# Performance work log

Hardware: AMD Instinct MI355X
Metric: run time of the kernel (lower is better)

## Reference

```python
import jax, jax.numpy as jnp
import numpy as np

# Static config mirroring FinalFFTAudioEngine(compression_ratio=0.3)
COMPRESSION_RATIO = 0.3
ENERGY_THRESHOLD = 0.05
WINDOW = 256  # window_size=512 -> power-of-2 loop ends at 512 -> min(512//2, 512) = 256


def _important_mask(energy, min_count, threshold):
    """Threshold mask, replaced by top-k mask if too few survive (faithful to torch code)."""
    th_mask = energy > threshold
    _, idx = jax.lax.top_k(energy, min_count)
    tk_mask = jnp.zeros(energy.shape, dtype=bool).at[idx].set(True)
    return jnp.where(jnp.sum(th_mask) < min_count, tk_mask, th_mask)


def setup_inputs() -> dict:
    key = jax.random.key(0)
    weight_matrix = jax.random.normal(key, (4096, 4096), dtype=jnp.float32)
    return {"weight_matrix": weight_matrix}


def reference(weight_matrix):
    # weight_to_audio_signal: flatten + max-abs normalize
    signal = weight_matrix.reshape(-1).astype(jnp.float32)
    n = signal.shape[0]  # 16777216, exact multiple of WINDOW -> no padding branch
    sig_max = jnp.max(jnp.abs(signal))
    norm = jnp.where(sig_max > 1e-10, sig_max, jnp.float32(1.0))
    signal = signal / norm

    # optimized_spectral_analysis: non-overlapping windows + per-window FFT
    windows = signal.reshape(-1, WINDOW)          # [T, F] = [65536, 256]
    spec = jnp.fft.fft(windows)                   # complex64 [T, F]

    # intelligent_frequency_selection
    energy = jnp.abs(spec) ** 2                   # [T, F]
    freq_energy = jnp.mean(energy, axis=0)        # [F]
    time_energy = jnp.mean(energy, axis=1)        # [T]
    min_freqs = max(1, int(WINDOW * (1.0 - COMPRESSION_RATIO * 0.7)))          # 202
    min_times = max(1, int(windows.shape[0] * (1.0 - COMPRESSION_RATIO * 0.7)))  # 51773
    freq_mask = _important_mask(freq_energy, min_freqs,
                                ENERGY_THRESHOLD * jnp.max(freq_energy))
    time_mask = _important_mask(time_energy, min_times,
                                ENERGY_THRESHOLD * jnp.max(time_energy))

    # lossless_compression: fused masked copy (replaces nested python double-for-loop)
    mask2d = time_mask[:, None] & freq_mask[None, :]
    compressed = jnp.where(mask2d, spec, jnp.zeros((), dtype=spec.dtype))

    # perfect_reconstruction: IFFT, take real part, flatten, trim to original length
    recon = jnp.real(jnp.fft.ifft(compressed)).reshape(-1)[:n]
    return recon
```

## Files before the change

kernel.cpp:

```cpp
#include <hip/hip_runtime.h>

#define N_TOTAL   16777216
#define NWIN      65536
#define MIN_FREQS 202
#define MIN_TIMES 51773
#define NSLOTS    64
#define NBLK      1024

#define IDX_TCNT    2
#define IDX_FMALL   3
#define IDX_TTHR    4
#define IDX_INVNORM 5
#define IDX_FCNT    6
#define IDX_FMASK   8
#define IDX_SLOTS   264
#define IDX_AMAXB   16648
#define IDX_TMAXB   18696
#define IDX_SUMSQ   20744
#define IDX_TMASKA  86280

__device__ __forceinline__ void fft16(float ar[16], float ai[16])
{
#define SWP(a,b) { float t_=ar[a]; ar[a]=ar[b]; ar[b]=t_; \
                   t_=ai[a]; ai[a]=ai[b]; ai[b]=t_; }
    SWP(1,8) SWP(2,4) SWP(3,12) SWP(5,10) SWP(7,14) SWP(11,13)
#undef SWP
#pragma unroll
    for (int i = 0; i < 16; i += 2) {
        float tr = ar[i+1], ti = ai[i+1];
        ar[i+1] = ar[i] - tr; ai[i+1] = ai[i] - ti;
        ar[i] += tr;          ai[i] += ti;
    }
#pragma unroll
    for (int i = 0; i < 16; i += 4) {
        { float tr = ar[i+2], ti = ai[i+2];
          ar[i+2] = ar[i] - tr; ai[i+2] = ai[i] - ti; ar[i] += tr; ai[i] += ti; }
        { float tr = ai[i+3], ti = -ar[i+3];
          ar[i+3] = ar[i+1] - tr; ai[i+3] = ai[i+1] - ti; ar[i+1] += tr; ai[i+1] += ti; }
    }
#pragma unroll
    for (int i = 0; i < 16; i += 8) {
        { float tr = ar[i+4], ti = ai[i+4];
          ar[i+4] = ar[i] - tr; ai[i+4] = ai[i] - ti; ar[i] += tr; ai[i] += ti; }
        { float br = ar[i+5], bi = ai[i+5];
          float tr = 0.70710678f * (br + bi), ti = 0.70710678f * (bi - br);
          ar[i+5] = ar[i+1] - tr; ai[i+5] = ai[i+1] - ti; ar[i+1] += tr; ai[i+1] += ti; }
        { float tr = ai[i+6], ti = -ar[i+6];
          ar[i+6] = ar[i+2] - tr; ai[i+6] = ai[i+2] - ti; ar[i+2] += tr; ai[i+2] += ti; }
        { float br = ar[i+7], bi = ai[i+7];
          float tr = 0.70710678f * (bi - br), ti = -0.70710678f * (br + bi);
          ar[i+7] = ar[i+3] - tr; ai[i+7] = ai[i+3] - ti; ar[i+3] += tr; ai[i+3] += ti; }
    }
    { float tr = ar[8], ti = ai[8];
      ar[8] = ar[0] - tr; ai[8] = ai[0] - ti; ar[0] += tr; ai[0] += ti; }
#define BUT(J, WR, WI) { float br = ar[8+J], bi = ai[8+J];     \
      float tr = br*(WR) - bi*(WI), ti = br*(WI) + bi*(WR);    \
      ar[8+J] = ar[J] - tr; ai[8+J] = ai[J] - ti; ar[J] += tr; ai[J] += ti; }
    BUT(1,  0.92387953f, -0.38268343f)
    BUT(2,  0.70710678f, -0.70710678f)
    BUT(3,  0.38268343f, -0.92387953f)
    BUT(4,  0.f, -1.f)
    BUT(5, -0.38268343f, -0.92387953f)
    BUT(6, -0.70710678f, -0.70710678f)
    BUT(7, -0.92387953f, -0.38268343f)
#undef BUT
}

__global__ __launch_bounds__(256) void k_stats(const float* __restrict__ x,
                                               float* __restrict__ W)
{
    __shared__ float B[16][272];
    __shared__ float sE[256];
    __shared__ float red[256];
    const int tid  = threadIdx.x;
    const int lane = tid & 63;
    const int wv   = tid >> 6;
    const int subw = lane >> 4;
    const int n2   = lane & 15;
    float* Bs = B[wv * 4 + subw];

    float cs, sn;
    __sincosf(-0.024543692606170f * (float)n2, &sn, &cs);

    float e[16];
#pragma unroll
    for (int k = 0; k < 16; ++k) e[k] = 0.f;
    float amax = 0.f, tmx = 0.f;
    float* sumsq = W + IDX_SUMSQ;

    const int wave_gid = (blockIdx.x << 2) | wv;
    const int GSTRIDE  = 4 * NBLK;

    const float4* xg = (const float4*)(x + (size_t)wave_gid * 1024);
    float4 v0 = xg[lane];
    float4 v1 = xg[64 + lane];
    float4 v2 = xg[128 + lane];
    float4 v3 = xg[192 + lane];

#pragma unroll 1
    for (int g = wave_gid; g < NWIN / 4; g += GSTRIDE) {
        *(float4*)&B[wv * 4 + 0][lane * 4] = v0;
        *(float4*)&B[wv * 4 + 1][lane * 4] = v1;
        *(float4*)&B[wv * 4 + 2][lane * 4] = v2;
        *(float4*)&B[wv * 4 + 3][lane * 4] = v3;
        amax = fmaxf(amax, fmaxf(fmaxf(fabsf(v0.x), fabsf(v0.y)),
                                 fmaxf(fabsf(v0.z), fabsf(v0.w))));
        amax = fmaxf(amax, fmaxf(fmaxf(fabsf(v1.x), fabsf(v1.y)),
                                 fmaxf(fabsf(v1.z), fabsf(v1.w))));
        amax = fmaxf(amax, fmaxf(fmaxf(fabsf(v2.x), fabsf(v2.y)),
                                 fmaxf(fabsf(v2.z), fabsf(v2.w))));
        amax = fmaxf(amax, fmaxf(fmaxf(fabsf(v3.x), fabsf(v3.y)),
                                 fmaxf(fabsf(v3.z), fabsf(v3.w))));
        const int gn = g + GSTRIDE;
        if (gn < NWIN / 4) {
            const float4* xn = (const float4*)(x + (size_t)gn * 1024);
            v0 = xn[lane];
            v1 = xn[64 + lane];
            v2 = xn[128 + lane];
            v3 = xn[192 + lane];
        }
        asm volatile("s_waitcnt lgkmcnt(0)" ::: "memory");
        __builtin_amdgcn_sched_barrier(0);
        float ar[16], ai[16];
#pragma unroll
        for (int j = 0; j < 16; ++j) { ar[j] = Bs[16 * j + n2]; ai[j] = 0.f; }

        fft16(ar, ai);

        { float wr = 1.f, wi = 0.f;
#pragma unroll
          for (int k = 1; k < 16; ++k) {
              const float nwr = wr * cs - wi * sn;
              const float nwi = wr * sn + wi * cs;
              wr = nwr; wi = nwi;
              const float xr = ar[k], xi = ai[k];
              ar[k] = xr * wr - xi * wi;
              ai[k] = xr * wi + xi * wr;
          } }

#pragma unroll
        for (int k = 0; k < 16; ++k) Bs[17 * k + n2] = ar[k];
        asm volatile("s_waitcnt lgkmcnt(0)" ::: "memory");
        __builtin_amdgcn_sched_barrier(0);
#pragma unroll
        for (int k = 0; k < 16; ++k) ar[k] = Bs[17 * n2 + k];
        asm volatile("" ::: "memory");
#pragma unroll
        for (int k = 0; k < 16; ++k) Bs[17 * k + n2] = ai[k];
        asm volatile("s_waitcnt lgkmcnt(0)" ::: "memory");
        __builtin_amdgcn_sched_barrier(0);
#pragma unroll
        for (int k = 0; k < 16; ++k) ai[k] = Bs[17 * n2 + k];

        fft16(ar, ai);

        float p = 0.f;
#pragma unroll
        for (int k = 0; k < 16; ++k) {
            const float t = fmaf(ar[k], ar[k], ai[k] * ai[k]);
            e[k] += t; p += t;
        }
        p += __shfl_xor(p, 1); p += __shfl_xor(p, 2);
        p += __shfl_xor(p, 4); p += __shfl_xor(p, 8);
        if (n2 == 0) sumsq[g * 4 + subw] = p;
        tmx = fmaxf(tmx, p);
    }

    sE[tid] = 0.f;
    __syncthreads();
#pragma unroll
    for (int k = 0; k < 16; ++k)
        atomicAdd(&sE[k * 16 + n2], e[k]);
    __syncthreads();
    atomicAdd(&W[IDX_SLOTS + (size_t)(blockIdx.x & (NSLOTS - 1)) * 256 + tid], sE[tid]);

    red[tid] = amax; __syncthreads();
    for (int s = 128; s > 0; s >>= 1) {
        if (tid < s) red[tid] = fmaxf(red[tid], red[tid + s]);
        __syncthreads();
    }
    if (tid == 0) W[IDX_AMAXB + blockIdx.x] = red[0];
    __syncthreads();
    red[tid] = tmx; __syncthreads();
    for (int s = 128; s > 0; s >>= 1) {
        if (tid < s) red[tid] = fmaxf(red[tid], red[tid + s]);
        __syncthreads();
    }
    if (tid == 0) W[IDX_TMAXB + blockIdx.x] = red[0];
}

__global__ __launch_bounds__(256) void k_masks(float* __restrict__ W)
{
    __shared__ float e[256];
    __shared__ float red[256];
    const int tid = threadIdx.x;
    float am = 0.f, tm = 0.f;
#pragma unroll
    for (int k = 0; k < NBLK / 256; ++k) {
        am = fmaxf(am, W[IDX_AMAXB + k * 256 + tid]);
        tm = fmaxf(tm, W[IDX_TMAXB + k * 256 + tid]);
    }
    red[tid] = am; __syncthreads();
    for (int s = 128; s > 0; s >>= 1) {
        if (tid < s) red[tid] = fmaxf(red[tid], red[tid + s]);
        __syncthreads();
    }
    const float amax = red[0];
    __syncthreads();
    red[tid] = tm; __syncthreads();
    for (int s = 128; s > 0; s >>= 1) {
        if (tid < s) red[tid] = fmaxf(red[tid], red[tid + s]);
        __syncthreads();
    }
    const float tmax = red[0];
    __syncthreads();

    float acc = 0.f;
#pragma unroll
    for (int s = 0; s < NSLOTS; s++) acc += W[IDX_SLOTS + s * 256 + tid];
    e[tid] = acc;
    red[tid] = acc; __syncthreads();
    for (int s = 128; s > 0; s >>= 1) {
        if (tid < s) red[tid] = fmaxf(red[tid], red[tid + s]);
        __syncthreads();
    }
    const float fthr = 0.05f * red[0];
    __syncthreads();
    const int my = (acc > fthr) ? 1 : 0;
    red[tid] = (float)my; __syncthreads();
    for (int s = 128; s > 0; s >>= 1) {
        if (tid < s) red[tid] += red[tid + s];
        __syncthreads();
    }
    const int fcnt = (int)red[0];
    __syncthreads();
    float m;
    if (fcnt >= MIN_FREQS) {
        m = (float)my;
    } else {
        int rank = 0;
        for (int j = 0; j < 256; j++) {
            const float ej = e[j];
            if (ej > acc || (ej == acc && j < tid)) rank++;
        }
        m = (rank < MIN_FREQS) ? 1.f : 0.f;
    }
    W[IDX_FMASK + tid] = m;
    red[tid] = m; __syncthreads();
    for (int s = 128; s > 0; s >>= 1) {
        if (tid < s) red[tid] += red[tid + s];
        __syncthreads();
    }
    if (tid == 0) {
        ((int*)W)[IDX_FMALL] = ((int)red[0] == 256) ? 1 : 0;
        ((int*)W)[IDX_FCNT]  = fcnt;
        W[IDX_INVNORM] = 1.f / ((amax > 1e-10f) ? amax : 1.f);
        W[IDX_TTHR] = 0.05f * tmax;
    }
}

__global__ __launch_bounds__(256) void k_tmask(float* __restrict__ W)
{
    __shared__ float red[256];
    const float tthr = W[IDX_TTHR];
    const float* sumsq = W + IDX_SUMSQ;
    float* tmask = W + IDX_TMASKA;
    const int base = blockIdx.x * 1024 + threadIdx.x;
    int c = 0;
#pragma unroll
    for (int k = 0; k < 4; k++) {
        const int i = base + k * 256;
        const int mm = (sumsq[i] > tthr) ? 1 : 0;
        c += mm;
        tmask[i] = (float)mm;
    }
    red[threadIdx.x] = (float)c; __syncthreads();
    for (int s = 128; s > 0; s >>= 1) {
        if (threadIdx.x < s) red[threadIdx.x] += red[threadIdx.x + s];
        __syncthreads();
    }
    if (threadIdx.x == 0) atomicAdd((int*)W + IDX_TCNT, (int)red[0]);
}

__global__ __launch_bounds__(256) void k_timefb(float* __restrict__ W)
{
    if (((const int*)W)[IDX_TCNT] >= MIN_TIMES) return;
    const int t = blockIdx.x * 256 + threadIdx.x;
    const float* sumsq = W + IDX_SUMSQ;
    const float st = sumsq[t];
    int rank = 0;
    for (int j = 0; j < NWIN; j++) {
        const float sj = sumsq[j];
        if (sj > st || (sj == st && j < t)) rank++;
    }
    W[IDX_TMASKA + t] = (rank < MIN_TIMES) ? 1.f : 0.f;
}

__global__ __launch_bounds__(256) void k_out(const float* __restrict__ x,
                                             float* __restrict__ out,
                                             const float* __restrict__ W)
{
    const int tid = threadIdx.x;
    const int fm_all = ((const int*)W)[IDX_FMALL];
    const float inv_norm = W[IDX_INVNORM];
    if (fm_all) {
        const float4* xi = (const float4*)x;
        float4* yo = (float4*)out;
        const float* tmask = W + IDX_TMASKA;
        for (int i = blockIdx.x * 256 + tid; i < N_TOTAL / 4; i += gridDim.x * 256) {
            const float s = inv_norm * tmask[i >> 6];
            float4 v = xi[i];
            v.x *= s; v.y *= s; v.z *= s; v.w *= s;
            yo[i] = v;
        }
        return;
    }
    __shared__ float re[256], im[256], twr[128], twi[128], fm[256];
    if (tid < 128) {
        float s, c;
        __sincosf(-6.283185307179586f * (float)tid / 256.0f, &s, &c);
        twr[tid] = c; twi[tid] = s;
    }
    fm[tid] = W[IDX_FMASK + (int)(__brev((unsigned)tid) >> 24)];
    __syncthreads();
    const float scale = inv_norm * (1.f / 256.f);
    for (int w = blockIdx.x; w < NWIN; w += gridDim.x) {
        const float tm = W[IDX_TMASKA + w];
        if (tm == 0.f) { out[w * 256 + tid] = 0.f; continue; }
        re[tid] = x[w * 256 + tid]; im[tid] = 0.f;
        __syncthreads();
        for (int lh = 7; lh >= 0; lh--) {
            const int half = 1 << lh;
            if (tid < 128) {
                const int k  = tid & (half - 1);
                const int i0 = ((tid & ~(half - 1)) << 1) | k;
                const int i1 = i0 + half;
                const float ar = re[i0], ai = im[i0], br = re[i1], bi = im[i1];
                const float dr = ar - br, di = ai - bi;
                re[i0] = ar + br; im[i0] = ai + bi;
                const int ti = k << (7 - lh);
                const float wr = twr[ti], wi = twi[ti];
                re[i1] = dr * wr - di * wi;
                im[i1] = dr * wi + di * wr;
            }
            __syncthreads();
        }
        re[tid] *= fm[tid]; im[tid] *= fm[tid];
        __syncthreads();
        for (int lh = 0; lh < 8; lh++) {
            const int half = 1 << lh;
            if (tid < 128) {
                const int k  = tid & (half - 1);
                const int i0 = ((tid & ~(half - 1)) << 1) | k;
                const int i1 = i0 + half;
                const int ti = k << (7 - lh);
                const float wr = twr[ti], wi = -twi[ti];
                const float br = re[i1], bi = im[i1];
                const float tr = br * wr - bi * wi;
                const float ts = br * wi + bi * wr;
                const float ar = re[i0], ai = im[i0];
                re[i1] = ar - tr; im[i1] = ai - ts;
                re[i0] = ar + tr; im[i0] = ai + ts;
            }
            __syncthreads();
        }
        out[w * 256 + tid] = re[tid] * scale;
        __syncthreads();
    }
}

extern "C" void kernel_launch(void* const* d_in, const int* in_sizes, int n_in,
                              void* d_out, int out_size, void* d_ws, size_t ws_size,
                              hipStream_t stream)
{
    const float* x = (const float*)d_in[0];
    float* out = (float*)d_out;
    float* W = (float*)d_ws;
    hipMemsetAsync(d_ws, 0, (size_t)IDX_AMAXB * sizeof(float), stream);
    hipLaunchKernelGGL(k_stats,  dim3(NBLK), dim3(256), 0, stream, x, W);
    hipLaunchKernelGGL(k_masks,  dim3(1),    dim3(256), 0, stream, W);
    hipLaunchKernelGGL(k_tmask,  dim3(64),   dim3(256), 0, stream, W);
    hipLaunchKernelGGL(k_timefb, dim3(256),  dim3(256), 0, stream, W);
    hipLaunchKernelGGL(k_out,    dim3(2048), dim3(256), 0, stream, x, out, W);
}
```

Baseline: 84.47 us.

## Merge mask kernels, precompute twiddles, use float2 LDS transpose and DPP reductions

Merges the single-block frequency-mask kernel and the time-mask kernel into one 65-block launch, where the time-mask blocks each recompute the global time maximum instead of waiting for a separate kernel. In k_stats, per-lane twiddles are precomputed into registers outside the loop, and the real/imag LDS transpose becomes a single float2 pass. The four-step 16-lane shuffle sum becomes DPP row operations. This cuts one launch, redundant twiddle arithmetic and LDS round trips, at the cost of more registers, a larger shared buffer, and redundant max reductions across 64 blocks.

Measured after the change: 128.4 us. +52.0%, slower.

```diff
diff --git a/kernel.cpp b/kernel.cpp
--- a/kernel.cpp
+++ b/kernel.cpp
@@ -18,6 +18,15 @@
 #define IDX_TMAXB   18696
 #define IDX_SUMSQ   20744
 #define IDX_TMASKA  86280
+
+__device__ __forceinline__ float dpp_row_sum16(float x)
+{
+    x += __int_as_float(__builtin_amdgcn_mov_dpp(__float_as_int(x), 0xB1,  0xF, 0xF, true));
+    x += __int_as_float(__builtin_amdgcn_mov_dpp(__float_as_int(x), 0x4E,  0xF, 0xF, true));
+    x += __int_as_float(__builtin_amdgcn_mov_dpp(__float_as_int(x), 0x141, 0xF, 0xF, true));
+    x += __int_as_float(__builtin_amdgcn_mov_dpp(__float_as_int(x), 0x140, 0xF, 0xF, true));
+    return x;
+}
 
 __device__ __forceinline__ void fft16(float ar[16], float ai[16])
 {
@@ -66,10 +75,10 @@
 #undef BUT
 }
 
-__global__ __launch_bounds__(256) void k_stats(const float* __restrict__ x,
-                                               float* __restrict__ W)
-{
-    __shared__ float B[16][272];
+__global__ __launch_bounds__(256, 4) void k_stats(const float* __restrict__ x,
+                                                  float* __restrict__ W)
+{
+    __shared__ float B[16][552];
     __shared__ float sE[256];
     __shared__ float red[256];
     const int tid  = threadIdx.x;
@@ -78,9 +87,19 @@
     const int subw = lane >> 4;
     const int n2   = lane & 15;
     float* Bs = B[wv * 4 + subw];
-
-    float cs, sn;
-    __sincosf(-0.024543692606170f * (float)n2, &sn, &cs);
+    float2* Bs2 = (float2*)Bs;
+
+    float twr[16], twi[16];
+    {
+        float cs, sn;
+        __sincosf(-0.024543692606170f * (float)n2, &sn, &cs);
+        twr[0] = 1.f; twi[0] = 0.f;
+#pragma unroll
+        for (int k = 1; k < 16; ++k) {
+            twr[k] = twr[k-1] * cs - twi[k-1] * sn;
+            twi[k] = twr[k-1] * sn + twi[k-1] * cs;
+        }
+    }
 
     float e[16];
 #pragma unroll
@@ -127,30 +146,23 @@
 
         fft16(ar, ai);
 
-        { float wr = 1.f, wi = 0.f;
-#pragma unroll
-          for (int k = 1; k < 16; ++k) {
-              const float nwr = wr * cs - wi * sn;
-              const float nwi = wr * sn + wi * cs;
-              wr = nwr; wi = nwi;
-              const float xr = ar[k], xi = ai[k];
-              ar[k] = xr * wr - xi * wi;
-              ai[k] = xr * wi + xi * wr;
-          } }
-
-#pragma unroll
-        for (int k = 0; k < 16; ++k) Bs[17 * k + n2] = ar[k];
+#pragma unroll
+        for (int k = 1; k < 16; ++k) {
+            const float xr = ar[k], xi = ai[k];
+            ar[k] = xr * twr[k] - xi * twi[k];
+            ai[k] = xr * twi[k] + xi * twr[k];
+        }
+
+#pragma unroll
+        for (int k = 0; k < 16; ++k)
+            Bs2[17 * k + n2] = make_float2(ar[k], ai[k]);
         asm volatile("s_waitcnt lgkmcnt(0)" ::: "memory");
         __builtin_amdgcn_sched_barrier(0);
 #pragma unroll
-        for (int k = 0; k < 16; ++k) ar[k] = Bs[17 * n2 + k];
-        asm volatile("" ::: "memory");
-#pragma unroll
-        for (int k = 0; k < 16; ++k) Bs[17 * k + n2] = ai[k];
-        asm volatile("s_waitcnt lgkmcnt(0)" ::: "memory");
-        __builtin_amdgcn_sched_barrier(0);
-#pragma unroll
-        for (int k = 0; k < 16; ++k) ai[k] = Bs[17 * n2 + k];
+        for (int k = 0; k < 16; ++k) {
+            const float2 t = Bs2[17 * n2 + k];
+            ar[k] = t.x; ai[k] = t.y;
+        }
 
         fft16(ar, ai);
 
@@ -160,8 +172,7 @@
             const float t = fmaf(ar[k], ar[k], ai[k] * ai[k]);
             e[k] += t; p += t;
         }
-        p += __shfl_xor(p, 1); p += __shfl_xor(p, 2);
-        p += __shfl_xor(p, 4); p += __shfl_xor(p, 8);
+        p = dpp_row_sum16(p);
         if (n2 == 0) sumsq[g * 4 + subw] = p;
         tmx = fmaxf(tmx, p);
     }
@@ -189,30 +200,54 @@
     if (tid == 0) W[IDX_TMAXB + blockIdx.x] = red[0];
 }
 
-__global__ __launch_bounds__(256) void k_masks(float* __restrict__ W)
-{
-    __shared__ float e[256];
+__global__ __launch_bounds__(256) void k_post(float* __restrict__ W)
+{
     __shared__ float red[256];
     const int tid = threadIdx.x;
-    float am = 0.f, tm = 0.f;
-#pragma unroll
-    for (int k = 0; k < NBLK / 256; ++k) {
+
+    if (blockIdx.x != 0) {
+        float tm = 0.f;
+#pragma unroll
+        for (int k = 0; k < NBLK / 256; ++k)
+            tm = fmaxf(tm, W[IDX_TMAXB + k * 256 + tid]);
+        red[tid] = tm; __syncthreads();
+        for (int s = 128; s > 0; s >>= 1) {
+            if (tid < s) red[tid] = fmaxf(red[tid], red[tid + s]);
+            __syncthreads();
+        }
+        const float tthr = 0.05f * red[0];
+        __syncthreads();
+        const float* sumsq = W + IDX_SUMSQ;
+        float* tmask = W + IDX_TMASKA;
+        const int base = (blockIdx.x - 1) * 1024 + tid;
+        int c = 0;
+#pragma unroll
+        for (int k = 0; k < 4; k++) {
+            const int i = base + k * 256;
+            const int mm = (sumsq[i] > tthr) ? 1 : 0;
+            c += mm;
+            tmask[i] = (float)mm;
+        }
+        red[tid] = (float)c; __syncthreads();
+        for (int s = 128; s > 0; s >>= 1) {
+            if (tid < s) red[tid] += red[tid + s];
+            __syncthreads();
+        }
+        if (tid == 0) atomicAdd((int*)W + IDX_TCNT, (int)red[0]);
+        return;
+    }
+
+    __shared__ float e[256];
+    float am = 0.f;
+#pragma unroll
+    for (int k = 0; k < NBLK / 256; ++k)
         am = fmaxf(am, W[IDX_AMAXB + k * 256 + tid]);
-        tm = fmaxf(tm, W[IDX_TMAXB + k * 256 + tid]);
-    }
     red[tid] = am; __syncthreads();
     for (int s = 128; s > 0; s >>= 1) {
         if (tid < s) red[tid] = fmaxf(red[tid], red[tid + s]);
         __syncthreads();
     }
     const float amax = red[0];
-    __syncthreads();
-    red[tid] = tm; __syncthreads();
-    for (int s = 128; s > 0; s >>= 1) {
-        if (tid < s) red[tid] = fmaxf(red[tid], red[tid + s]);
-        __syncthreads();
-    }
-    const float tmax = red[0];
     __syncthreads();
 
     float acc = 0.f;
@@ -255,31 +290,7 @@
         ((int*)W)[IDX_FMALL] = ((int)red[0] == 256) ? 1 : 0;
         ((int*)W)[IDX_FCNT]  = fcnt;
         W[IDX_INVNORM] = 1.f / ((amax > 1e-10f) ? amax : 1.f);
-        W[IDX_TTHR] = 0.05f * tmax;
-    }
-}
-
-__global__ __launch_bounds__(256) void k_tmask(float* __restrict__ W)
-{
-    __shared__ float red[256];
-    const float tthr = W[IDX_TTHR];
-    const float* sumsq = W + IDX_SUMSQ;
-    float* tmask = W + IDX_TMASKA;
-    const int base = blockIdx.x * 1024 + threadIdx.x;
-    int c = 0;
-#pragma unroll
-    for (int k = 0; k < 4; k++) {
-        const int i = base + k * 256;
-        const int mm = (sumsq[i] > tthr) ? 1 : 0;
-        c += mm;
-        tmask[i] = (float)mm;
-    }
-    red[threadIdx.x] = (float)c; __syncthreads();
-    for (int s = 128; s > 0; s >>= 1) {
-        if (threadIdx.x < s) red[threadIdx.x] += red[threadIdx.x + s];
-        __syncthreads();
-    }
-    if (threadIdx.x == 0) atomicAdd((int*)W + IDX_TCNT, (int)red[0]);
+    }
 }
 
 __global__ __launch_bounds__(256) void k_timefb(float* __restrict__ W)
@@ -378,8 +389,7 @@
     float* W = (float*)d_ws;
     hipMemsetAsync(d_ws, 0, (size_t)IDX_AMAXB * sizeof(float), stream);
     hipLaunchKernelGGL(k_stats,  dim3(NBLK), dim3(256), 0, stream, x, W);
-    hipLaunchKernelGGL(k_masks,  dim3(1),    dim3(256), 0, stream, W);
-    hipLaunchKernelGGL(k_tmask,  dim3(64),   dim3(256), 0, stream, W);
+    hipLaunchKernelGGL(k_post,   dim3(65),   dim3(256), 0, stream, W);
     hipLaunchKernelGGL(k_timefb, dim3(256),  dim3(256), 0, stream, W);
     hipLaunchKernelGGL(k_out,    dim3(2048), dim3(256), 0, stream, x, out, W);
 }
```
